# Kernel optimization log

Measured on AMD Instinct MI355X. Metric: run time of the kernel, lower is better.

Reference implementation:

```python
import jax, jax.numpy as jnp
import numpy as np

N, E = 16384, 262144
NS_N, NV_N = 128, 64      # node irreps: 128x0e + 64x1o
NS_E, NV_E = 64, 32       # edge irreps: 64x0e + 32x1o
C_OH, LAT = 16, 128
DS, DV = 128, 64          # irreps_out: 128x0e + 64x1o
GS = DS + DV              # gate input scalars (128 act scalars + 64 gates)
SC = 2 * NS_N + NS_E      # 320 concatenated scalar channels
VC = 2 * NV_N + NV_E      # 160 concatenated l=1 channels
M0_IN = SC + VC           # 480 m=0 features into SO2 linear
M0_OUT = GS + DV          # 256 m=0 outputs
AVG_NEI = 16.0
EPS = 1e-8


def setup_inputs() -> dict:
    key = jax.random.key(0)
    ks = jax.random.split(key, 20)
    f = lambda k, s: jax.random.normal(k, s, dtype=jnp.float32)
    return dict(
        node_feat=f(ks[0], (N, NS_N + 3 * NV_N)),
        edge_feat=f(ks[1], (E, NS_E + 3 * NV_E)),
        edge_vec=f(ks[2], (E, 3)),
        latents=f(ks[3], (E, LAT)),
        node_onehot=jax.nn.one_hot(jax.random.randint(ks[4], (N,), 0, C_OH), C_OH, dtype=jnp.float32),
        ln_n_g0=jnp.ones(NS_N), ln_n_b0=jnp.zeros(NS_N), ln_n_g1=jnp.ones(NV_N),
        ln_e_g0=jnp.ones(NS_E), ln_e_b0=jnp.zeros(NS_E), ln_e_g1=jnp.ones(NV_E),
        W_m0=f(ks[5], (M0_IN, M0_OUT)),
        w_r=f(ks[6], (VC, DV)), w_i=f(ks[7], (VC, DV)),
        W_env=f(ks[8], (LAT, DS + DV)),
        Wp0=f(ks[9], (DS, DS)), bp0=jnp.zeros(DS), Wpv=f(ks[10], (DV, DV)),
        Wtp0=f(ks[11], (DS, C_OH, GS)), Wtp1=f(ks[12], (DV, C_OH, DV)),
        Wo0=f(ks[13], (DS, DS)), bo0=jnp.zeros(DS), Wov=f(ks[14], (DV, DV)),
        res_param=jnp.zeros(()),
        edge_index=jax.random.randint(ks[15], (2, E), 0, N),
    )


def _sep_ln(s, v, g0, b0, g1):
    # separable equivariant layer norm: LN on scalars, per-sample RMS on l=1 block
    mu = s.mean(-1, keepdims=True)
    var = jnp.mean((s - mu) ** 2, -1, keepdims=True)
    s = (s - mu) * jax.lax.rsqrt(var + EPS) * g0 + b0
    vvar = jnp.mean(v * v, axis=(-2, -1), keepdims=True)  # component norm, degree-balanced (single l=1)
    v = v * jax.lax.rsqrt(vvar + EPS) * g1[None, :, None]
    return s, v


def _edge_frame(vec):
    # orthonormal frame (a, e1, e2) with a along the edge
    a = vec * jax.lax.rsqrt(jnp.sum(vec * vec, -1, keepdims=True) + EPS)
    helper = jnp.where(jnp.abs(a[:, 2:3]) < 0.99,
                       jnp.array([0.0, 0.0, 1.0], dtype=vec.dtype),
                       jnp.array([1.0, 0.0, 0.0], dtype=vec.dtype))
    e1 = jnp.cross(helper, a)
    e1 = e1 * jax.lax.rsqrt(jnp.sum(e1 * e1, -1, keepdims=True) + EPS)
    e2 = jnp.cross(a, e1)
    return a, e1, e2


def reference(node_feat, edge_feat, edge_vec, latents, node_onehot,
              ln_n_g0, ln_n_b0, ln_n_g1, ln_e_g0, ln_e_b0, ln_e_g1,
              W_m0, w_r, w_i, W_env, Wp0, bp0, Wpv,
              Wtp0, Wtp1, Wo0, bo0, Wov, res_param, edge_index):
    src, dst = edge_index[0], edge_index[1]
    ns, nv = node_feat[:, :NS_N], node_feat[:, NS_N:].reshape(-1, NV_N, 3)
    es, ev = edge_feat[:, :NS_E], edge_feat[:, NS_E:].reshape(-1, NV_E, 3)
    ns, nv = _sep_ln(ns, nv, ln_n_g0, ln_n_b0, ln_n_g1)
    es, ev = _sep_ln(es, ev, ln_e_g0, ln_e_b0, ln_e_g1)
    # per-edge concat: node[src] + edge + node[dst]
    s_cat = jnp.concatenate([ns[src], es, ns[dst]], -1)          # [E, SC]
    v_cat = jnp.concatenate([nv[src], ev, nv[dst]], 1)           # [E, VC, 3]
    # SO2 linear: rotate into edge frame, mix per |m|, rotate back
    a, e1, e2 = _edge_frame(edge_vec)
    c0 = jnp.einsum('eci,ei->ec', v_cat, a)
    c1 = jnp.einsum('eci,ei->ec', v_cat, e1)
    c2 = jnp.einsum('eci,ei->ec', v_cat, e2)
    m0 = jnp.concatenate([s_cat, c0], -1) @ W_m0 * (1.0 / np.sqrt(M0_IN))  # [E, M0_OUT]
    s_out, c0o = m0[:, :GS], m0[:, GS:]
    inv = 1.0 / np.sqrt(VC)
    c1o = (c1 @ w_r - c2 @ w_i) * inv
    c2o = (c1 @ w_i + c2 @ w_r) * inv
    v_out = (c0o[..., None] * a[:, None, :] + c1o[..., None] * e1[:, None, :]
             + c2o[..., None] * e2[:, None, :])                  # [E, DV, 3]
    # gate activation
    s_act = jax.nn.silu(s_out[:, :DS])
    gates = jax.nn.sigmoid(s_out[:, DS:])
    v_g = v_out * gates[..., None]
    # lin_post (per-l linear, scalar bias)
    s2 = s_act @ Wp0 * (1.0 / np.sqrt(DS)) + bp0
    v2 = jnp.einsum('eui,uv->evi', v_g, Wpv) * (1.0 / np.sqrt(DV))
    # env weighting from latents (E3ElementLinear, per-irrep-channel scalars)
    w = latents @ W_env * (1.0 / np.sqrt(LAT))
    s2 = s2 * w[:, :DS]
    v2 = v2 * w[:, DS:, None]
    nrm = 1.0 / np.sqrt(AVG_NEI)
    sa = jax.ops.segment_sum(s2, dst, num_segments=N) * nrm
    va = jax.ops.segment_sum(v2, dst, num_segments=N) * nrm
    # one-hot FullyConnectedTensorProduct (in2 all 0e) + gate + linear
    t0 = jnp.einsum('nu,nc,ucv->nv', sa, node_onehot, Wtp0) * (1.0 / np.sqrt(DS * C_OH))
    t1 = jnp.einsum('nui,nc,ucv->nvi', va, node_onehot, Wtp1) * (1.0 / np.sqrt(DV * C_OH))
    s3 = jax.nn.silu(t0[:, :DS])
    v3 = t1 * jax.nn.sigmoid(t0[:, DS:])[..., None]
    s4 = s3 @ Wo0 * (1.0 / np.sqrt(DS)) + bo0
    v4 = jnp.einsum('nui,uv->nvi', v3, Wov) * (1.0 / np.sqrt(DV))
    new = jnp.concatenate([s4, v4.reshape(-1, 3 * DV)], -1)
    r = jax.nn.sigmoid(res_param)
    return r * node_feat + (1.0 - r) * new
```

## Files before the change

kernel.cpp:

```cpp
#include <hip/hip_runtime.h>
#include <math.h>

#define N_NODES 16384
#define N_EDGES 262144
#define EPSF 1e-8f

#define OFF_X     0
#define OFF_C12   31232
#define OFF_FR    52224
#define OFF_EDST  52992
#define POOL_BYTES 53120
#define OFF_SACT  0
#define OFF_GATE  8704
#define OFF_C0O   17408
#define OFF_C1O   31232
#define OFF_C2O   39936
#define OFF_VG    8704

typedef __bf16 bf16x8 __attribute__((ext_vector_type(8)));
typedef float  f32x4  __attribute__((ext_vector_type(4)));

__device__ __forceinline__ f32x4 MFMA16(bf16x8 a, bf16x8 b, f32x4 c){
  return __builtin_amdgcn_mfma_f32_16x16x32_bf16(a, b, c, 0, 0, 0);
}

__device__ __forceinline__ unsigned short f2bf(float x){
  __bf16 h = (__bf16)x;
  union { __bf16 b; unsigned short u; } c; c.b = h;
  return c.u;
}
__device__ __forceinline__ float bf2f(unsigned short h){
  union { unsigned u; float f; } c; c.u = ((unsigned)h)<<16;
  return c.f;
}
__device__ __forceinline__ float wsum64(float v){
  #pragma unroll
  for (int m=1; m<64; m<<=1) v += __shfl_xor(v, m);
  return v;
}
__device__ __forceinline__ float wsum32(float v){
  #pragma unroll
  for (int m=1; m<32; m<<=1) v += __shfl_xor(v, m);
  return v;
}
__device__ __forceinline__ float sigm(float x){ return 1.0f/(1.0f+__expf(-x)); }
__device__ __forceinline__ float silu(float x){ return x/(1.0f+__expf(-x)); }

__global__ __launch_bounds__(256) void k_pack_all(
  const float* __restrict__ Wm0, const float* __restrict__ wr,
  const float* __restrict__ wi,  const float* __restrict__ Wenv,
  const float* __restrict__ Wp0, const float* __restrict__ Wpv,
  unsigned short* __restrict__ wpk)
{
  int i = blockIdx.x*256 + threadIdx.x;
  if (i < 122880){
    int k = i >> 8, n = i & 255;
    int idx = (((k>>5)*256 + n)*4 + ((k>>3)&3))*8 + (k&7);
    wpk[idx] = f2bf(Wm0[i]);
  } else if (i < 163840){
    int j = i - 122880;
    int k = j >> 7, n = j & 127;
    float v;
    if (k < 160) v = (n < 64) ? wr[k*64 + n]        : wi[k*64 + (n-64)];
    else         v = (n < 64) ? -wi[(k-160)*64 + n] : wr[(k-160)*64 + (n-64)];
    int idx = (((k>>5)*128 + n)*4 + ((k>>3)&3))*8 + (k&7);
    wpk[122880 + idx] = f2bf(v);
  } else if (i < 188416){
    int j = i - 163840;
    int k = j / 192, n = j - k*192;
    int idx = (((k>>5)*192 + n)*4 + ((k>>3)&3))*8 + (k&7);
    wpk[163840 + idx] = f2bf(Wenv[j]);
  } else if (i < 204800){
    int j = i - 188416;
    int k = j >> 7, n = j & 127;
    int idx = (((k>>5)*128 + n)*4 + ((k>>3)&3))*8 + (k&7);
    wpk[188416 + idx] = f2bf(Wp0[j]);
  } else if (i < 208896){
    int j = i - 204800;
    int k = j >> 6, n = j & 63;
    int idx = (((k>>5)*64 + n)*4 + ((k>>3)&3))*8 + (k&7);
    wpk[204800 + idx] = f2bf(Wpv[j]);
  }
}

__global__ __launch_bounds__(256) void k_hist(const int* __restrict__ eidx, int* __restrict__ cnt){
  int e = blockIdx.x*256 + threadIdx.x;
  if (e < N_EDGES) atomicAdd(&cnt[eidx[N_EDGES+e]], 1);
}
__global__ __launch_bounds__(256) void k_scan(const int* __restrict__ cnt,
                                              int* __restrict__ rowp, int* __restrict__ cursor){
  __shared__ int part[256];
  __shared__ int pref[257];
  const int t = threadIdx.x;
  const int base = t*64;
  int s = 0;
  for (int i=0;i<64;i++) s += cnt[base+i];
  part[t] = s; __syncthreads();
  if (t==0){ int a=0; for (int i=0;i<256;i++){ pref[i]=a; a+=part[i]; } pref[256]=a; }
  __syncthreads();
  int a = pref[t];
  for (int i=0;i<64;i++){ rowp[base+i]=a; cursor[base+i]=a; a += cnt[base+i]; }
  if (t==0) rowp[N_NODES] = pref[256];
}
__global__ __launch_bounds__(256) void k_fill(const int* __restrict__ eidx,
                                              int* __restrict__ cursor, int* __restrict__ perm){
  int e = blockIdx.x*256 + threadIdx.x;
  if (e < N_EDGES){
    int pos = atomicAdd(&cursor[eidx[N_EDGES+e]], 1);
    perm[pos] = e;
  }
}

__global__ __launch_bounds__(256) void k_node_ln(
    const float* __restrict__ nf, const float* __restrict__ g0,
    const float* __restrict__ b0, const float* __restrict__ g1,
    unsigned short* __restrict__ ns_ln, _Float16* __restrict__ nv_ln)
{
  const int tid  = threadIdx.x;
  const int lane = tid & 63;
  const int n    = blockIdx.x*4 + (tid>>6);
  const float* row = nf + (size_t)n*320;

  float s0 = row[lane], s1 = row[64+lane];
  float mu = wsum64(s0+s1) * (1.0f/128.0f);
  float d0 = s0-mu, d1 = s1-mu;
  float var = wsum64(d0*d0+d1*d1) * (1.0f/128.0f);
  float rs = rsqrtf(var + EPSF);
  ns_ln[(size_t)n*128 + lane]    = f2bf(d0*rs*g0[lane]    + b0[lane]);
  ns_ln[(size_t)n*128 + 64+lane] = f2bf(d1*rs*g0[64+lane] + b0[64+lane]);

  float px = row[128+lane*3+0], py = row[128+lane*3+1], pz = row[128+lane*3+2];
  float vvar = wsum64(px*px+py*py+pz*pz) * (1.0f/192.0f);
  float vsc = rsqrtf(vvar + EPSF) * g1[lane];
  nv_ln[(size_t)n*192 + lane*3+0] = (_Float16)(px*vsc);
  nv_ln[(size_t)n*192 + lane*3+1] = (_Float16)(py*vsc);
  nv_ln[(size_t)n*192 + lane*3+2] = (_Float16)(pz*vsc);
}

__global__ __launch_bounds__(256) void k_wenv(
  const float* __restrict__ lats, const unsigned short* __restrict__ pWenv,
  const int* __restrict__ perm, unsigned short* __restrict__ wbuf)
{
  __shared__ unsigned short A[64*136];
  const int tid = threadIdx.x;
  {
    const int row = tid>>2, part = tid&3;
    const int slot = blockIdx.x*64 + row;
    const int e = perm[slot];
    const float* lr = lats + (size_t)e*128 + part*32;
    #pragma unroll
    for (int q=0;q<8;q++){
      float4 v = *(const float4*)(lr + q*4);
      int cb = part*32 + q*4;
      A[row*136 + cb+0] = f2bf(v.x);
      A[row*136 + cb+1] = f2bf(v.y);
      A[row*136 + cb+2] = f2bf(v.z);
      A[row*136 + cb+3] = f2bf(v.w);
    }
  }
  __syncthreads();
  const int wid = tid>>6, l = tid&63, r15 = l&15, g = l>>4;
  const f32x4 zero4 = {0.f,0.f,0.f,0.f};
  f32x4 acc[4][3];
  #pragma unroll
  for (int m=0;m<4;m++)
    #pragma unroll
    for (int n=0;n<3;n++) acc[m][n]=zero4;

  const unsigned short* bbase = pWenv + ((size_t)(wid*48 + r15)*4 + g)*8;
  #pragma unroll
  for (int kc=0;kc<4;kc++){
    bf16x8 b[3];
    #pragma unroll
    for (int n=0;n<3;n++) b[n] = *(const bf16x8*)(bbase + (size_t)kc*6144 + n*512);
    #pragma unroll
    for (int m=0;m<4;m++){
      bf16x8 a = *(const bf16x8*)&A[(m*16+r15)*136 + kc*32 + g*8];
      #pragma unroll
      for (int n=0;n<3;n++) acc[m][n] = MFMA16(a, b[n], acc[m][n]);
    }
  }
  #pragma unroll
  for (int m=0;m<4;m++)
    #pragma unroll
    for (int n=0;n<3;n++)
      #pragma unroll
      for (int r=0;r<4;r++){
        int sr = m*16 + g*4 + r;
        int j  = wid*48 + n*16 + r15;
        wbuf[(size_t)(blockIdx.x*64 + sr)*192 + j] = f2bf(acc[m][n][r]*0.08838834764831845f);
      }
}

__global__ __launch_bounds__(256,3) void k_edge(
  const float* __restrict__ ef, const float* __restrict__ evec,
  const float* __restrict__ g0e, const float* __restrict__ b0e, const float* __restrict__ g1e,
  const unsigned short* __restrict__ pWm0, const unsigned short* __restrict__ pWc,
  const unsigned short* __restrict__ pWp0, const unsigned short* __restrict__ pWpv,
  const float* __restrict__ bp0,
  const int* __restrict__ eidx, const int* __restrict__ perm,
  const unsigned short* __restrict__ ns_ln, const _Float16* __restrict__ nv_ln,
  const unsigned short* __restrict__ wbuf,
  float* __restrict__ sa, float* __restrict__ va)
{
  extern __shared__ unsigned char pool[];
  const int tid = threadIdx.x;
  unsigned short* Xs   = (unsigned short*)(pool + OFF_X);
  unsigned short* C12s = (unsigned short*)(pool + OFF_C12);
  _Float16* FRh = (_Float16*)(pool + OFF_FR);
  int*   EDST = (int*)(pool + OFF_EDST);

  const int wid = tid>>6, l = tid&63;
  const int r15 = l&15, g = l>>4;

  const int sbase = blockIdx.x*32;
  float wsc[2][2][4], wvc[2][4], bp0v[2];
  #pragma unroll
  for (int n=0;n<2;n++) bp0v[n] = bp0[wid*32 + n*16 + r15];
  #pragma unroll
  for (int m=0;m<2;m++)
    #pragma unroll
    for (int r=0;r<4;r++){
      int e = m*16 + g*4 + r;
      #pragma unroll
      for (int n=0;n<2;n++)
        wsc[m][n][r] = bf2f(wbuf[(size_t)(sbase+e)*192 + wid*32 + n*16 + r15]);
      wvc[m][r] = bf2f(wbuf[(size_t)(sbase+e)*192 + 128 + wid*16 + r15]);
    }

  {
    const int ln = tid & 31;
    #pragma unroll
    for (int eo=0; eo<4; ++eo){
      const int el = eo*8 + (tid>>5);
      const int slot = blockIdx.x*32 + el;
      const size_t e = (size_t)perm[slot];
      const int src = eidx[e];
      const int dst = eidx[N_EDGES + e];

      float vx=evec[e*3+0], vy=evec[e*3+1], vz=evec[e*3+2];
      float rn = rsqrtf(vx*vx+vy*vy+vz*vz+EPSF);
      float ax=vx*rn, ay=vy*rn, az=vz*rn;
      float hx, hz;
      if (fabsf(az) < 0.99f){ hx=0.f; hz=1.f; } else { hx=1.f; hz=0.f; }
      float e1x = -hz*ay;
      float e1y = hz*ax - hx*az;
      float e1z = hx*ay;
      float rn1 = rsqrtf(e1x*e1x+e1y*e1y+e1z*e1z+EPSF);
      e1x*=rn1; e1y*=rn1; e1z*=rn1;
      float e2x = ay*e1z - az*e1y;
      float e2y = az*e1x - ax*e1z;
      float e2z = ax*e1y - ay*e1x;
      if (ln==0){
        FRh[el*12+0]=(_Float16)ax;  FRh[el*12+1]=(_Float16)ay;  FRh[el*12+2]=(_Float16)az;
        FRh[el*12+3]=(_Float16)e1x; FRh[el*12+4]=(_Float16)e1y; FRh[el*12+5]=(_Float16)e1z;
        FRh[el*12+6]=(_Float16)e2x; FRh[el*12+7]=(_Float16)e2y; FRh[el*12+8]=(_Float16)e2z;
        EDST[el]=dst;
      }

      const float* erow = ef + e*160;
      float s0=erow[ln], s1=erow[32+ln];
      float mu = wsum32(s0+s1)*(1.f/64.f);
      float d0=s0-mu, d1=s1-mu;
      float var = wsum32(d0*d0+d1*d1)*(1.f/64.f);
      float rs = rsqrtf(var+EPSF);
      Xs[el*488 + 128+ln] = f2bf(d0*rs*g0e[ln]    + b0e[ln]);
      Xs[el*488 + 160+ln] = f2bf(d1*rs*g0e[32+ln] + b0e[32+ln]);

      float wx=erow[64+ln*3+0], wy=erow[64+ln*3+1], wz=erow[64+ln*3+2];
      float vvar = wsum32(wx*wx+wy*wy+wz*wz)*(1.f/96.f);
      float vsc = rsqrtf(vvar+EPSF)*g1e[ln];
      wx*=vsc; wy*=vsc; wz*=vsc;
      Xs  [el*488 + 320+64+ln]   = f2bf(wx*ax +wy*ay +wz*az);
      C12s[el*328 + 64+ln]       = f2bf(wx*e1x+wy*e1y+wz*e1z);
      C12s[el*328 + 160+64+ln]   = f2bf(wx*e2x+wy*e2y+wz*e2z);

      const unsigned short* nss = ns_ln + (size_t)src*128;
      const unsigned short* nsd = ns_ln + (size_t)dst*128;
      *(uint2*)&Xs[el*488 + ln*4]       = *(const uint2*)&nss[ln*4];
      *(uint2*)&Xs[el*488 + 192 + ln*4] = *(const uint2*)&nsd[ln*4];

      const _Float16* nvs = nv_ln + (size_t)src*192;
      const _Float16* nvd = nv_ln + (size_t)dst*192;
      #pragma unroll
      for (int q=0;q<2;q++){
        int u = ln+32*q;
        float px=(float)nvs[u*3+0], py=(float)nvs[u*3+1], pz=(float)nvs[u*3+2];
        Xs  [el*488 + 320+u]     = f2bf(px*ax +py*ay +pz*az);
        C12s[el*328 + u]         = f2bf(px*e1x+py*e1y+pz*e1z);
        C12s[el*328 + 160+u]     = f2bf(px*e2x+py*e2y+pz*e2z);
        px=(float)nvd[u*3+0]; py=(float)nvd[u*3+1]; pz=(float)nvd[u*3+2];
        Xs  [el*488 + 320+96+u]  = f2bf(px*ax +py*ay +pz*az);
        C12s[el*328 + 96+u]      = f2bf(px*e1x+py*e1y+pz*e1z);
        C12s[el*328 + 160+96+u]  = f2bf(px*e2x+py*e2y+pz*e2z);
      }
    }
  }
  __syncthreads();

  const f32x4 zero4 = {0.f,0.f,0.f,0.f};

  f32x4 acc1[2][4], acc2[2][2];
  #pragma unroll
  for (int m=0;m<2;m++){
    #pragma unroll
    for (int n=0;n<4;n++) acc1[m][n]=zero4;
    #pragma unroll
    for (int n=0;n<2;n++) acc2[m][n]=zero4;
  }

  {
    const unsigned short* bbase = pWm0 + ((size_t)(wid*64 + r15)*4 + g)*8;
    bf16x8 bc[4];
    #pragma unroll
    for (int n=0;n<4;n++) bc[n] = *(const bf16x8*)(bbase + n*512);
    for (int kc=0;kc<15;kc++){
      bf16x8 a0 = *(const bf16x8*)&Xs[(    r15)*488 + kc*32 + g*8];
      bf16x8 a1 = *(const bf16x8*)&Xs[(16+ r15)*488 + kc*32 + g*8];
      bf16x8 bn[4];
      if (kc<14){
        const unsigned short* np = bbase + (size_t)(kc+1)*8192;
        #pragma unroll
        for (int n=0;n<4;n++) bn[n] = *(const bf16x8*)(np + n*512);
      }
      #pragma unroll
      for (int n=0;n<4;n++){
        acc1[0][n] = MFMA16(a0,bc[n],acc1[0][n]);
        acc1[1][n] = MFMA16(a1,bc[n],acc1[1][n]);
      }
      #pragma unroll
      for (int n=0;n<4;n++) bc[n]=bn[n];
    }
  }
  {
    const unsigned short* bbase = pWc + ((size_t)(wid*32 + r15)*4 + g)*8;
    bf16x8 bc[2];
    #pragma unroll
    for (int n=0;n<2;n++) bc[n] = *(const bf16x8*)(bbase + n*512);
    for (int kc=0;kc<10;kc++){
      bf16x8 a0 = *(const bf16x8*)&C12s[(    r15)*328 + kc*32 + g*8];
      bf16x8 a1 = *(const bf16x8*)&C12s[(16+ r15)*328 + kc*32 + g*8];
      bf16x8 bn[2];
      if (kc<9){
        const unsigned short* np = bbase + (size_t)(kc+1)*4096;
        #pragma unroll
        for (int n=0;n<2;n++) bn[n] = *(const bf16x8*)(np + n*512);
      }
      #pragma unroll
      for (int n=0;n<2;n++){
        acc2[0][n] = MFMA16(a0,bc[n],acc2[0][n]);
        acc2[1][n] = MFMA16(a1,bc[n],acc2[1][n]);
      }
      #pragma unroll
      for (int n=0;n<2;n++) bc[n]=bn[n];
    }
  }

  __syncthreads();

  {
    unsigned short* SAs = (unsigned short*)(pool + OFF_SACT);
    float* GAf = (float*)(pool + OFF_GATE);
    float* C0f = (float*)(pool + OFF_C0O);
    #pragma unroll
    for (int m=0;m<2;m++)
      #pragma unroll
      for (int n=0;n<4;n++)
        #pragma unroll
        for (int r=0;r<4;r++){
          int e = m*16 + g*4 + r;
          int j = wid*64 + n*16 + r15;
          float v = acc1[m][n][r]*0.04564354645876384f;
          if (j < 128)      SAs[e*136 + j] = f2bf(silu(v));
          else if (j < 192) GAf[e*68 + (j-128)] = sigm(v);
          else              C0f[e*68 + (j-192)] = v;
        }
    float* C1f = (float*)(pool + OFF_C1O);
    float* C2f = (float*)(pool + OFF_C2O);
    #pragma unroll
    for (int m=0;m<2;m++)
      #pragma unroll
      for (int n=0;n<2;n++)
        #pragma unroll
        for (int r=0;r<4;r++){
          int e = m*16 + g*4 + r;
          int j = wid*32 + n*16 + r15;
          float v = acc2[m][n][r]*0.07905694150420949f;
          if (j < 64) C1f[e*68 + j] = v;
          else        C2f[e*68 + (j-64)] = v;
        }
  }
  __syncthreads();

  {
    const int e = tid>>3, u0 = (tid&7)*8;
    const float* GAf = (const float*)(pool + OFF_GATE);
    const float* C0f = (const float*)(pool + OFF_C0O);
    const float* C1f = (const float*)(pool + OFF_C1O);
    const float* C2f = (const float*)(pool + OFF_C2O);
    float ax=(float)FRh[e*12+0],  ay=(float)FRh[e*12+1],  az=(float)FRh[e*12+2];
    float b1x=(float)FRh[e*12+3], b1y=(float)FRh[e*12+4], b1z=(float)FRh[e*12+5];
    float b2x=(float)FRh[e*12+6], b2y=(float)FRh[e*12+7], b2z=(float)FRh[e*12+8];
    float vgx[8], vgy[8], vgz[8];
    #pragma unroll
    for (int i=0;i<8;i++){
      int u = u0+i;
      float gt = GAf[e*68+u];
      float c0 = C0f[e*68+u], c1 = C1f[e*68+u], c2 = C2f[e*68+u];
      vgx[i] = (c0*ax + c1*b1x + c2*b2x)*gt;
      vgy[i] = (c0*ay + c1*b1y + c2*b2y)*gt;
      vgz[i] = (c0*az + c1*b1z + c2*b2z)*gt;
    }
    __syncthreads();
    unsigned short* VGs = (unsigned short*)(pool + OFF_VG);
    #pragma unroll
    for (int i=0;i<8;i++){
      VGs[0*2304 + e*72 + u0+i] = f2bf(vgx[i]);
      VGs[1*2304 + e*72 + u0+i] = f2bf(vgy[i]);
      VGs[2*2304 + e*72 + u0+i] = f2bf(vgz[i]);
    }
  }
  __syncthreads();

  {
    const unsigned short* SAs = (const unsigned short*)(pool + OFF_SACT);
    const unsigned short* VGs = (const unsigned short*)(pool + OFF_VG);

    f32x4 acc4[2][2], acc5[3][2];
    #pragma unroll
    for (int m=0;m<2;m++){ acc4[m][0]=zero4; acc4[m][1]=zero4; }
    #pragma unroll
    for (int c=0;c<3;c++){ acc5[c][0]=zero4; acc5[c][1]=zero4; }

    {
      const unsigned short* bbase = pWp0 + ((size_t)(wid*32 + r15)*4 + g)*8;
      #pragma unroll
      for (int kc=0;kc<4;kc++){
        bf16x8 a0 = *(const bf16x8*)&SAs[(    r15)*136 + kc*32 + g*8];
        bf16x8 a1 = *(const bf16x8*)&SAs[(16+ r15)*136 + kc*32 + g*8];
        #pragma unroll
        for (int n=0;n<2;n++){
          bf16x8 b = *(const bf16x8*)(bbase + (size_t)kc*4096 + n*512);
          acc4[0][n] = MFMA16(a0,b,acc4[0][n]);
          acc4[1][n] = MFMA16(a1,b,acc4[1][n]);
        }
      }
    }
    {
      bf16x8 b5[2];
      #pragma unroll
      for (int kc=0;kc<2;kc++)
        b5[kc] = *(const bf16x8*)(pWpv + ((size_t)(kc*64 + wid*16 + r15)*4 + g)*8);
      #pragma unroll
      for (int c=0;c<3;c++)
        #pragma unroll
        for (int kc=0;kc<2;kc++){
          bf16x8 a0 = *(const bf16x8*)&VGs[c*2304 + (    r15)*72 + kc*32 + g*8];
          bf16x8 a1 = *(const bf16x8*)&VGs[c*2304 + (16+ r15)*72 + kc*32 + g*8];
          acc5[c][0] = MFMA16(a0,b5[kc],acc5[c][0]);
          acc5[c][1] = MFMA16(a1,b5[kc],acc5[c][1]);
        }
    }

    __syncthreads();
    float* R = (float*)pool;
    #pragma unroll
    for (int m=0;m<2;m++)
      #pragma unroll
      for (int n=0;n<2;n++)
        #pragma unroll
        for (int r=0;r<4;r++){
          int e = m*16 + g*4 + r;
          int j = wid*32 + n*16 + r15;
          R[e*320 + j] = (acc4[m][n][r]*0.08838834764831845f + bp0v[n]) * wsc[m][n][r];
        }
    #pragma unroll
    for (int c=0;c<3;c++)
      #pragma unroll
      for (int m=0;m<2;m++)
        #pragma unroll
        for (int r=0;r<4;r++){
          int e = m*16 + g*4 + r;
          int vch = wid*16 + r15;
          R[e*320 + 128 + vch*3 + c] = acc5[c][m][r]*0.125f * wvc[m][r];
        }
    __syncthreads();

    for (int j = tid; j < 320; j += 256){
      float accv = R[j];
      int cur = EDST[0];
      for (int e=1;e<32;e++){
        int d = EDST[e];
        float v = R[e*320 + j];
        if (d != cur){
          float* tgt = (j<128) ? &sa[(size_t)cur*128 + j] : &va[(size_t)cur*192 + (j-128)];
          atomicAdd(tgt, accv);
          accv = v; cur = d;
        } else accv += v;
      }
      float* tgt = (j<128) ? &sa[(size_t)cur*128 + j] : &va[(size_t)cur*192 + (j-128)];
      atomicAdd(tgt, accv);
    }
  }
}

__global__ __launch_bounds__(256) void k_node_out(
  const float* __restrict__ nf, const float* __restrict__ oh,
  const float* __restrict__ Wtp0, const float* __restrict__ Wtp1,
  const float* __restrict__ Wo0, const float* __restrict__ bo0,
  const float* __restrict__ Wov, const float* __restrict__ resp,
  const float* __restrict__ sa, const float* __restrict__ va,
  float* __restrict__ out)
{
  __shared__ float SAB[4][128];
  __shared__ float VX[4][64], VY[4][64], VZ[4][64];
  __shared__ float S3 [4][128];
  __shared__ float V3 [4][256];
  const int tid=threadIdx.x, lane=tid&63, g=tid>>6;
  const int n = blockIdx.x*4 + g;

  float cf=0.f;
  #pragma unroll
  for (int j=0;j<16;j++) cf += j*oh[(size_t)n*16+j];
  const int c = (int)(cf+0.5f);

  SAB[g][lane]    = sa[(size_t)n*128+lane]   *0.25f;
  SAB[g][64+lane] = sa[(size_t)n*128+64+lane]*0.25f;
  VX[g][lane] = va[(size_t)n*192+lane*3+0]*0.25f;
  VY[g][lane] = va[(size_t)n*192+lane*3+1]*0.25f;
  VZ[g][lane] = va[(size_t)n*192+lane*3+2]*0.25f;
  __syncthreads();

  float t00=0.f, t01=0.f, t02=0.f;
  const float* w0c = Wtp0 + (size_t)c*192;
  for (int u=0;u<128;u++){
    float s = SAB[g][u];
    t00 += s * w0c[(size_t)u*3072 + lane];
    t01 += s * w0c[(size_t)u*3072 + lane+64];
    t02 += s * w0c[(size_t)u*3072 + lane+128];
  }
  const float sct0 = 0.02209708691f;
  t00*=sct0; t01*=sct0; t02*=sct0;

  float t1x=0.f,t1y=0.f,t1z=0.f;
  const float* w1c = Wtp1 + (size_t)c*64;
  for (int u=0;u<64;u++){
    float wv = w1c[(size_t)u*1024 + lane];
    t1x += VX[g][u]*wv;
    t1y += VY[g][u]*wv;
    t1z += VZ[g][u]*wv;
  }
  t1x*=0.03125f; t1y*=0.03125f; t1z*=0.03125f;

  S3[g][lane]    = silu(t00);
  S3[g][64+lane] = silu(t01);
  float g2 = sigm(t02);
  float4 v3v = {t1x*g2, t1y*g2, t1z*g2, 0.f};
  *(float4*)&V3[g][lane*4] = v3v;
  __syncthreads();

  float s40=0.f, s41=0.f;
  for (int k=0;k<128;k++){
    float s3k = S3[g][k];
    s40 += s3k*Wo0[k*128+lane];
    s41 += s3k*Wo0[k*128+64+lane];
  }
  s40 = s40*0.08838834765f + bo0[lane];
  s41 = s41*0.08838834765f + bo0[64+lane];

  float v4x=0.f,v4y=0.f,v4z=0.f;
  for (int u=0;u<64;u++){
    float4 v3u = *(const float4*)&V3[g][u*4];
    float wv = Wov[u*64+lane];
    v4x += v3u.x*wv; v4y += v3u.y*wv; v4z += v3u.z*wv;
  }
  v4x*=0.125f; v4y*=0.125f; v4z*=0.125f;

  const float r = sigm(resp[0]);
  const float* row = nf + (size_t)n*320;
  float* orow = out + (size_t)n*320;
  orow[lane]      = r*row[lane]      + (1.f-r)*s40;
  orow[64+lane]   = r*row[64+lane]   + (1.f-r)*s41;
  orow[128+lane*3+0] = r*row[128+lane*3+0] + (1.f-r)*v4x;
  orow[128+lane*3+1] = r*row[128+lane*3+1] + (1.f-r)*v4y;
  orow[128+lane*3+2] = r*row[128+lane*3+2] + (1.f-r)*v4z;
}

extern "C" void kernel_launch(void* const* d_in, const int* in_sizes, int n_in,
                              void* d_out, int out_size, void* d_ws, size_t ws_size,
                              hipStream_t stream)
{
  const float* nf   = (const float*)d_in[0];
  const float* ef   = (const float*)d_in[1];
  const float* evec = (const float*)d_in[2];
  const float* lats = (const float*)d_in[3];
  const float* oh   = (const float*)d_in[4];
  const float* g0n  = (const float*)d_in[5];
  const float* b0n  = (const float*)d_in[6];
  const float* g1n  = (const float*)d_in[7];
  const float* g0e  = (const float*)d_in[8];
  const float* b0e  = (const float*)d_in[9];
  const float* g1e  = (const float*)d_in[10];
  const float* Wm0  = (const float*)d_in[11];
  const float* wr   = (const float*)d_in[12];
  const float* wi   = (const float*)d_in[13];
  const float* Wenv = (const float*)d_in[14];
  const float* Wp0  = (const float*)d_in[15];
  const float* bp0  = (const float*)d_in[16];
  const float* Wpv  = (const float*)d_in[17];
  const float* Wtp0 = (const float*)d_in[18];
  const float* Wtp1 = (const float*)d_in[19];
  const float* Wo0  = (const float*)d_in[20];
  const float* bo0  = (const float*)d_in[21];
  const float* Wov  = (const float*)d_in[22];
  const float* resp = (const float*)d_in[23];
  const int*   eidx = (const int*)d_in[24];

  char* base = (char*)d_ws;
  unsigned short* ns_ln = (unsigned short*)(base);
  _Float16* nv_ln = (_Float16*)(base + 4194304);
  float* sa    = (float*)(base + 10485760);
  float* va    = (float*)(base + 18874368);
  unsigned short* wpk = (unsigned short*)(base + 31457280);
  unsigned short* pWm0  = wpk;
  unsigned short* pWc   = wpk + 122880;
  unsigned short* pWenv = wpk + 163840;
  unsigned short* pWp0  = wpk + 188416;
  unsigned short* pWpv  = wpk + 204800;
  int* ibuf   = (int*)(base + 31875072);
  int* cnt    = ibuf;
  int* rowp   = ibuf + 16384;
  int* cursor = ibuf + 32769;
  int* perm   = ibuf + 49153;
  unsigned short* wbuf = (unsigned short*)(base + 33120264);

  hipMemsetAsync(sa, 0, (size_t)N_NODES*320*sizeof(float), stream);
  hipMemsetAsync(cnt, 0, N_NODES*sizeof(int), stream);

  k_pack_all<<<(208896+255)/256, 256, 0, stream>>>(Wm0, wr, wi, Wenv, Wp0, Wpv, wpk);
  k_node_ln<<<N_NODES/4, 256, 0, stream>>>(nf, g0n, b0n, g1n, ns_ln, nv_ln);

  k_hist<<<(N_EDGES+255)/256, 256, 0, stream>>>(eidx, cnt);
  k_scan<<<1, 256, 0, stream>>>(cnt, rowp, cursor);
  k_fill<<<(N_EDGES+255)/256, 256, 0, stream>>>(eidx, cursor, perm);

  k_wenv<<<N_EDGES/64, 256, 0, stream>>>(lats, pWenv, perm, wbuf);

  k_edge<<<N_EDGES/32, 256, POOL_BYTES, stream>>>(ef, evec, g0e, b0e, g1e,
                                                  pWm0, pWc, pWp0, pWpv, bp0,
                                                  eidx, perm, ns_ln, nv_ln, wbuf,
                                                  sa, va);
  k_node_out<<<N_NODES/4, 256, 0, stream>>>(nf, oh, Wtp0, Wtp1, Wo0, bo0, Wov,
                                            resp, sa, va, (float*)d_out);
}
```

Baseline: 591.2 us.

## Shrink edge kernel LDS, gather node scalars into registers, raise occupancy

The node-scalar parts of the m=0 input are now gathered straight from global memory into MFMA A-operand registers instead of being staged in shared memory. The edge stage's gate, C0/C1/C2 and reduction buffers are stored as bf16/fp16 instead of fp32. Together these cut the LDS pool from about 53 KB to about 37 KB, and launch bounds go from 3 to 4 blocks per CU. Blocks are also swizzled across the grid and the wbuf loads move after the GEMMs, trading lower register and LDS pressure for reduced intermediate precision.

```diff
diff --git a/kernel.cpp b/kernel.cpp
--- a/kernel.cpp
+++ b/kernel.cpp
@@ -5,16 +5,17 @@
 #define N_EDGES 262144
 #define EPSF 1e-8f
 
-#define OFF_X     0
-#define OFF_C12   31232
-#define OFF_FR    52224
-#define OFF_EDST  52992
-#define POOL_BYTES 53120
+#define OFF_XE    0
+#define OFF_C12   14848
+#define OFF_FR    35840
+#define OFF_EDST  36608
+#define OFF_ESRC  36736
+#define POOL_BYTES 36864
 #define OFF_SACT  0
 #define OFF_GATE  8704
-#define OFF_C0O   17408
-#define OFF_C1O   31232
-#define OFF_C2O   39936
+#define OFF_C0O   13312
+#define OFF_C1O   17920
+#define OFF_C2O   22528
 #define OFF_VG    8704
 
 typedef __bf16 bf16x8 __attribute__((ext_vector_type(8)));
@@ -192,7 +193,7 @@
       }
 }
 
-__global__ __launch_bounds__(256,3) void k_edge(
+__global__ __launch_bounds__(256,4) void k_edge(
   const float* __restrict__ ef, const float* __restrict__ evec,
   const float* __restrict__ g0e, const float* __restrict__ b0e, const float* __restrict__ g1e,
   const unsigned short* __restrict__ pWm0, const unsigned short* __restrict__ pWc,
@@ -205,35 +206,25 @@
 {
   extern __shared__ unsigned char pool[];
   const int tid = threadIdx.x;
-  unsigned short* Xs   = (unsigned short*)(pool + OFF_X);
+  unsigned short* XE   = (unsigned short*)(pool + OFF_XE);
   unsigned short* C12s = (unsigned short*)(pool + OFF_C12);
   _Float16* FRh = (_Float16*)(pool + OFF_FR);
-  int*   EDST = (int*)(pool + OFF_EDST);
+  int* EDST = (int*)(pool + OFF_EDST);
+  int* ESRC = (int*)(pool + OFF_ESRC);
+
+  const int nwg = gridDim.x;
+  const int bswz = (blockIdx.x & 7)*(nwg>>3) + (blockIdx.x >> 3);
 
   const int wid = tid>>6, l = tid&63;
   const int r15 = l&15, g = l>>4;
-
-  const int sbase = blockIdx.x*32;
-  float wsc[2][2][4], wvc[2][4], bp0v[2];
-  #pragma unroll
-  for (int n=0;n<2;n++) bp0v[n] = bp0[wid*32 + n*16 + r15];
-  #pragma unroll
-  for (int m=0;m<2;m++)
-    #pragma unroll
-    for (int r=0;r<4;r++){
-      int e = m*16 + g*4 + r;
-      #pragma unroll
-      for (int n=0;n<2;n++)
-        wsc[m][n][r] = bf2f(wbuf[(size_t)(sbase+e)*192 + wid*32 + n*16 + r15]);
-      wvc[m][r] = bf2f(wbuf[(size_t)(sbase+e)*192 + 128 + wid*16 + r15]);
-    }
+  const int sbase = bswz*32;
 
   {
     const int ln = tid & 31;
     #pragma unroll
     for (int eo=0; eo<4; ++eo){
       const int el = eo*8 + (tid>>5);
-      const int slot = blockIdx.x*32 + el;
+      const int slot = sbase + el;
       const size_t e = (size_t)perm[slot];
       const int src = eidx[e];
       const int dst = eidx[N_EDGES + e];
@@ -256,6 +247,7 @@
         FRh[el*12+3]=(_Float16)e1x; FRh[el*12+4]=(_Float16)e1y; FRh[el*12+5]=(_Float16)e1z;
         FRh[el*12+6]=(_Float16)e2x; FRh[el*12+7]=(_Float16)e2y; FRh[el*12+8]=(_Float16)e2z;
         EDST[el]=dst;
+        ESRC[el]=src;
       }
 
       const float* erow = ef + e*160;
@@ -264,21 +256,16 @@
       float d0=s0-mu, d1=s1-mu;
       float var = wsum32(d0*d0+d1*d1)*(1.f/64.f);
       float rs = rsqrtf(var+EPSF);
-      Xs[el*488 + 128+ln] = f2bf(d0*rs*g0e[ln]    + b0e[ln]);
-      Xs[el*488 + 160+ln] = f2bf(d1*rs*g0e[32+ln] + b0e[32+ln]);
+      XE[el*232 + ln]    = f2bf(d0*rs*g0e[ln]    + b0e[ln]);
+      XE[el*232 + 32+ln] = f2bf(d1*rs*g0e[32+ln] + b0e[32+ln]);
 
       float wx=erow[64+ln*3+0], wy=erow[64+ln*3+1], wz=erow[64+ln*3+2];
       float vvar = wsum32(wx*wx+wy*wy+wz*wz)*(1.f/96.f);
       float vsc = rsqrtf(vvar+EPSF)*g1e[ln];
       wx*=vsc; wy*=vsc; wz*=vsc;
-      Xs  [el*488 + 320+64+ln]   = f2bf(wx*ax +wy*ay +wz*az);
+      XE  [el*232 + 64+64+ln]    = f2bf(wx*ax +wy*ay +wz*az);
       C12s[el*328 + 64+ln]       = f2bf(wx*e1x+wy*e1y+wz*e1z);
       C12s[el*328 + 160+64+ln]   = f2bf(wx*e2x+wy*e2y+wz*e2z);
-
-      const unsigned short* nss = ns_ln + (size_t)src*128;
-      const unsigned short* nsd = ns_ln + (size_t)dst*128;
-      *(uint2*)&Xs[el*488 + ln*4]       = *(const uint2*)&nss[ln*4];
-      *(uint2*)&Xs[el*488 + 192 + ln*4] = *(const uint2*)&nsd[ln*4];
 
       const _Float16* nvs = nv_ln + (size_t)src*192;
       const _Float16* nvd = nv_ln + (size_t)dst*192;
@@ -286,11 +273,11 @@
       for (int q=0;q<2;q++){
         int u = ln+32*q;
         float px=(float)nvs[u*3+0], py=(float)nvs[u*3+1], pz=(float)nvs[u*3+2];
-        Xs  [el*488 + 320+u]     = f2bf(px*ax +py*ay +pz*az);
+        XE  [el*232 + 64+u]      = f2bf(px*ax +py*ay +pz*az);
         C12s[el*328 + u]         = f2bf(px*e1x+py*e1y+pz*e1z);
         C12s[el*328 + 160+u]     = f2bf(px*e2x+py*e2y+pz*e2z);
         px=(float)nvd[u*3+0]; py=(float)nvd[u*3+1]; pz=(float)nvd[u*3+2];
-        Xs  [el*488 + 320+96+u]  = f2bf(px*ax +py*ay +pz*az);
+        XE  [el*232 + 64+96+u]   = f2bf(px*ax +py*ay +pz*az);
         C12s[el*328 + 96+u]      = f2bf(px*e1x+py*e1y+pz*e1z);
         C12s[el*328 + 160+96+u]  = f2bf(px*e2x+py*e2y+pz*e2z);
       }
@@ -300,68 +287,92 @@
 
   const f32x4 zero4 = {0.f,0.f,0.f,0.f};
 
-  f32x4 acc1[2][4], acc2[2][2];
-  #pragma unroll
-  for (int m=0;m<2;m++){
+  f32x4 acc1[2][4];
+  #pragma unroll
+  for (int m=0;m<2;m++)
     #pragma unroll
     for (int n=0;n<4;n++) acc1[m][n]=zero4;
-    #pragma unroll
-    for (int n=0;n<2;n++) acc2[m][n]=zero4;
-  }
 
   {
     const unsigned short* bbase = pWm0 + ((size_t)(wid*64 + r15)*4 + g)*8;
-    bf16x8 bc[4];
-    #pragma unroll
-    for (int n=0;n<4;n++) bc[n] = *(const bf16x8*)(bbase + n*512);
-    for (int kc=0;kc<15;kc++){
-      bf16x8 a0 = *(const bf16x8*)&Xs[(    r15)*488 + kc*32 + g*8];
-      bf16x8 a1 = *(const bf16x8*)&Xs[(16+ r15)*488 + kc*32 + g*8];
-      bf16x8 bn[4];
-      if (kc<14){
-        const unsigned short* np = bbase + (size_t)(kc+1)*8192;
-        #pragma unroll
-        for (int n=0;n<4;n++) bn[n] = *(const bf16x8*)(np + n*512);
-      }
+    bf16x8 gA[2][8];
+    {
+      const int rs0 = ESRC[r15], rs1 = ESRC[16+r15];
+      const int rd0 = EDST[r15], rd1 = EDST[16+r15];
+      #pragma unroll
+      for (int q=0;q<4;q++){
+        gA[0][q]   = *(const bf16x8*)&ns_ln[(size_t)rs0*128 + q*32 + g*8];
+        gA[1][q]   = *(const bf16x8*)&ns_ln[(size_t)rs1*128 + q*32 + g*8];
+        gA[0][4+q] = *(const bf16x8*)&ns_ln[(size_t)rd0*128 + q*32 + g*8];
+        gA[1][4+q] = *(const bf16x8*)&ns_ln[(size_t)rd1*128 + q*32 + g*8];
+      }
+    }
+    #pragma unroll
+    for (int t=0;t<7;t++){
+      const int kc  = (t<2) ? (4+t) : (10 + t-2);
+      const int col = (t<2) ? (t*32) : (64 + (t-2)*32);
+      bf16x8 a0 = *(const bf16x8*)&XE[(    r15)*232 + col + g*8];
+      bf16x8 a1 = *(const bf16x8*)&XE[(16+ r15)*232 + col + g*8];
+      const unsigned short* bp = bbase + (size_t)kc*8192;
       #pragma unroll
       for (int n=0;n<4;n++){
-        acc1[0][n] = MFMA16(a0,bc[n],acc1[0][n]);
-        acc1[1][n] = MFMA16(a1,bc[n],acc1[1][n]);
-      }
-      #pragma unroll
-      for (int n=0;n<4;n++) bc[n]=bn[n];
-    }
-  }
+        bf16x8 b = *(const bf16x8*)(bp + n*512);
+        acc1[0][n] = MFMA16(a0,b,acc1[0][n]);
+        acc1[1][n] = MFMA16(a1,b,acc1[1][n]);
+      }
+    }
+    #pragma unroll
+    for (int t=0;t<8;t++){
+      const int kc = (t<4) ? t : (6 + t-4);
+      const unsigned short* bp = bbase + (size_t)kc*8192;
+      #pragma unroll
+      for (int n=0;n<4;n++){
+        bf16x8 b = *(const bf16x8*)(bp + n*512);
+        acc1[0][n] = MFMA16(gA[0][t],b,acc1[0][n]);
+        acc1[1][n] = MFMA16(gA[1][t],b,acc1[1][n]);
+      }
+    }
+  }
+
+  f32x4 acc2[2][2];
+  #pragma unroll
+  for (int m=0;m<2;m++){ acc2[m][0]=zero4; acc2[m][1]=zero4; }
   {
     const unsigned short* bbase = pWc + ((size_t)(wid*32 + r15)*4 + g)*8;
-    bf16x8 bc[2];
-    #pragma unroll
-    for (int n=0;n<2;n++) bc[n] = *(const bf16x8*)(bbase + n*512);
+    #pragma unroll
     for (int kc=0;kc<10;kc++){
       bf16x8 a0 = *(const bf16x8*)&C12s[(    r15)*328 + kc*32 + g*8];
       bf16x8 a1 = *(const bf16x8*)&C12s[(16+ r15)*328 + kc*32 + g*8];
-      bf16x8 bn[2];
-      if (kc<9){
-        const unsigned short* np = bbase + (size_t)(kc+1)*4096;
-        #pragma unroll
-        for (int n=0;n<2;n++) bn[n] = *(const bf16x8*)(np + n*512);
-      }
+      const unsigned short* bp = bbase + (size_t)kc*4096;
       #pragma unroll
       for (int n=0;n<2;n++){
-        acc2[0][n] = MFMA16(a0,bc[n],acc2[0][n]);
-        acc2[1][n] = MFMA16(a1,bc[n],acc2[1][n]);
-      }
-      #pragma unroll
-      for (int n=0;n<2;n++) bc[n]=bn[n];
-    }
-  }
+        bf16x8 b = *(const bf16x8*)(bp + n*512);
+        acc2[0][n] = MFMA16(a0,b,acc2[0][n]);
+        acc2[1][n] = MFMA16(a1,b,acc2[1][n]);
+      }
+    }
+  }
+
+  float wsc[2][2][4], wvc[2][4], bp0v[2];
+  #pragma unroll
+  for (int n=0;n<2;n++) bp0v[n] = bp0[wid*32 + n*16 + r15];
+  #pragma unroll
+  for (int m=0;m<2;m++)
+    #pragma unroll
+    for (int r=0;r<4;r++){
+      int e = m*16 + g*4 + r;
+      #pragma unroll
+      for (int n=0;n<2;n++)
+        wsc[m][n][r] = bf2f(wbuf[(size_t)(sbase+e)*192 + wid*32 + n*16 + r15]);
+      wvc[m][r] = bf2f(wbuf[(size_t)(sbase+e)*192 + 128 + wid*16 + r15]);
+    }
 
   __syncthreads();
 
   {
     unsigned short* SAs = (unsigned short*)(pool + OFF_SACT);
-    float* GAf = (float*)(pool + OFF_GATE);
-    float* C0f = (float*)(pool + OFF_C0O);
+    unsigned short* GAb = (unsigned short*)(pool + OFF_GATE);
+    unsigned short* C0b = (unsigned short*)(pool + OFF_C0O);
     #pragma unroll
     for (int m=0;m<2;m++)
       #pragma unroll
@@ -372,11 +383,11 @@
           int j = wid*64 + n*16 + r15;
           float v = acc1[m][n][r]*0.04564354645876384f;
           if (j < 128)      SAs[e*136 + j] = f2bf(silu(v));
-          else if (j < 192) GAf[e*68 + (j-128)] = sigm(v);
-          else              C0f[e*68 + (j-192)] = v;
+          else if (j < 192) GAb[e*72 + (j-128)] = f2bf(sigm(v));
+          else              C0b[e*72 + (j-192)] = f2bf(v);
         }
-    float* C1f = (float*)(pool + OFF_C1O);
-    float* C2f = (float*)(pool + OFF_C2O);
+    unsigned short* C1b = (unsigned short*)(pool + OFF_C1O);
+    unsigned short* C2b = (unsigned short*)(pool + OFF_C2O);
     #pragma unroll
     for (int m=0;m<2;m++)
       #pragma unroll
@@ -386,18 +397,18 @@
           int e = m*16 + g*4 + r;
           int j = wid*32 + n*16 + r15;
           float v = acc2[m][n][r]*0.07905694150420949f;
-          if (j < 64) C1f[e*68 + j] = v;
-          else        C2f[e*68 + (j-64)] = v;
+          if (j < 64) C1b[e*72 + j] = f2bf(v);
+          else        C2b[e*72 + (j-64)] = f2bf(v);
         }
   }
   __syncthreads();
 
   {
     const int e = tid>>3, u0 = (tid&7)*8;
-    const float* GAf = (const float*)(pool + OFF_GATE);
-    const float* C0f = (const float*)(pool + OFF_C0O);
-    const float* C1f = (const float*)(pool + OFF_C1O);
-    const float* C2f = (const float*)(pool + OFF_C2O);
+    const unsigned short* GAb = (const unsigned short*)(pool + OFF_GATE);
+    const unsigned short* C0b = (const unsigned short*)(pool + OFF_C0O);
+    const unsigned short* C1b = (const unsigned short*)(pool + OFF_C1O);
+    const unsigned short* C2b = (const unsigned short*)(pool + OFF_C2O);
     float ax=(float)FRh[e*12+0],  ay=(float)FRh[e*12+1],  az=(float)FRh[e*12+2];
     float b1x=(float)FRh[e*12+3], b1y=(float)FRh[e*12+4], b1z=(float)FRh[e*12+5];
     float b2x=(float)FRh[e*12+6], b2y=(float)FRh[e*12+7], b2z=(float)FRh[e*12+8];
@@ -405,8 +416,8 @@
     #pragma unroll
     for (int i=0;i<8;i++){
       int u = u0+i;
-      float gt = GAf[e*68+u];
-      float c0 = C0f[e*68+u], c1 = C1f[e*68+u], c2 = C2f[e*68+u];
+      float gt = bf2f(GAb[e*72+u]);
+      float c0 = bf2f(C0b[e*72+u]), c1 = bf2f(C1b[e*72+u]), c2 = bf2f(C2b[e*72+u]);
       vgx[i] = (c0*ax + c1*b1x + c2*b2x)*gt;
       vgy[i] = (c0*ay + c1*b1y + c2*b2y)*gt;
       vgz[i] = (c0*az + c1*b1z + c2*b2z)*gt;
@@ -463,7 +474,7 @@
     }
 
     __syncthreads();
-    float* R = (float*)pool;
+    _Float16* R = (_Float16*)pool;
     #pragma unroll
     for (int m=0;m<2;m++)
       #pragma unroll
@@ -472,7 +483,7 @@
         for (int r=0;r<4;r++){
           int e = m*16 + g*4 + r;
           int j = wid*32 + n*16 + r15;
-          R[e*320 + j] = (acc4[m][n][r]*0.08838834764831845f + bp0v[n]) * wsc[m][n][r];
+          R[e*320 + j] = (_Float16)((acc4[m][n][r]*0.08838834764831845f + bp0v[n]) * wsc[m][n][r]);
         }
     #pragma unroll
     for (int c=0;c<3;c++)
@@ -482,16 +493,16 @@
         for (int r=0;r<4;r++){
           int e = m*16 + g*4 + r;
           int vch = wid*16 + r15;
-          R[e*320 + 128 + vch*3 + c] = acc5[c][m][r]*0.125f * wvc[m][r];
+          R[e*320 + 128 + vch*3 + c] = (_Float16)(acc5[c][m][r]*0.125f * wvc[m][r]);
         }
     __syncthreads();
 
     for (int j = tid; j < 320; j += 256){
-      float accv = R[j];
+      float accv = (float)R[j];
       int cur = EDST[0];
       for (int e=1;e<32;e++){
         int d = EDST[e];
-        float v = R[e*320 + j];
+        float v = (float)R[e*320 + j];
         if (d != cur){
           float* tgt = (j<128) ? &sa[(size_t)cur*128 + j] : &va[(size_t)cur*192 + (j-128)];
           atomicAdd(tgt, accv);
```

Result: no change. 587.6 us (-0.6%).
